# Kernel optimization log

Hardware: AMD Instinct MI355X
Metric: run time of the kernel (lower is better)

## Reference

```python
import jax, jax.numpy as jnp
import numpy as np

DIM = 128
HEADS = DIM // 8      # mala uses dim//8 heads
HEAD_DIM = 8
HID = int(DIM * 2.66) # 340
B, H, W = 8, 128, 128


def _ln(x, w, b):
    # WithBias LayerNorm over channel dim of NCHW (per-pixel)
    mu = jnp.mean(x, axis=1, keepdims=True)
    var = jnp.mean((x - mu) ** 2, axis=1, keepdims=True)
    return (x - mu) / jnp.sqrt(var + 1e-5) * w[None, :, None, None] + b[None, :, None, None]


def _conv1x1(x, w):
    return jnp.einsum('bchw,oc->bohw', x, w)


def _dwconv(x, w, pad):
    return jax.lax.conv_general_dilated(
        x, w, (1, 1), ((pad, pad), (pad, pad)),
        dimension_numbers=('NCHW', 'OIHW', 'NCHW'),
        feature_group_count=x.shape[1])


def _rope(h, w, head_dim, dtype):
    angle = 1.0 / 10000 ** jnp.linspace(0.0, 1.0, head_dim // 4, dtype=dtype)
    angle = jnp.repeat(angle, 2)                                  # [d/2]
    ih = jnp.arange(h, dtype=dtype)[:, None] * angle[None, :]     # [h, d/2]
    iw = jnp.arange(w, dtype=dtype)[:, None] * angle[None, :]     # [w, d/2]
    d2 = head_dim // 2
    sin = jnp.concatenate([jnp.broadcast_to(jnp.sin(ih)[:, None, :], (h, w, d2)),
                           jnp.broadcast_to(jnp.sin(iw)[None, :, :], (h, w, d2))], -1)
    cos = jnp.concatenate([jnp.broadcast_to(jnp.cos(ih)[:, None, :], (h, w, d2)),
                           jnp.broadcast_to(jnp.cos(iw)[None, :, :], (h, w, d2))], -1)
    return sin.reshape(h * w, head_dim), cos.reshape(h * w, head_dim)


def _rot2(x):
    x1 = x[..., 0::2]
    x2 = x[..., 1::2]
    return jnp.stack([-x2, x1], axis=-1).reshape(x.shape)


def _theta_shift(x, sin, cos):
    return x * cos + _rot2(x) * sin


def setup_inputs() -> dict:
    key = jax.random.key(0)
    ks = jax.random.split(key, 8)
    f = jnp.float32
    return {
        'x': jax.random.normal(ks[0], (B, DIM, H, W), f),
        'ln1_w': jnp.ones((DIM,), f), 'ln1_b': jnp.zeros((DIM,), f),
        'qkvo_w': jax.random.normal(ks[1], (4 * DIM, DIM), f) * (DIM ** -0.5),
        'qkvo_b': jnp.zeros((4 * DIM,), f),
        'lepe_w': jax.random.normal(ks[2], (DIM, 1, 5, 5), f) * 0.2,
        'lepe_b': jnp.zeros((DIM,), f),
        'proj_w': jax.random.normal(ks[3], (DIM, DIM), f) * (DIM ** -0.5),
        'proj_b': jnp.zeros((DIM,), f),
        'ln2_w': jnp.ones((DIM,), f), 'ln2_b': jnp.zeros((DIM,), f),
        'ffn_in_w': jax.random.normal(ks[4], (2 * HID, DIM), f) * (DIM ** -0.5),
        'ffn_dw_w': jax.random.normal(ks[5], (2 * HID, 1, 3, 3), f) * (1.0 / 3.0),
        'ffn_out_w': jax.random.normal(ks[6], (DIM, HID), f) * (HID ** -0.5),
    }


def reference(x, ln1_w, ln1_b, qkvo_w, qkvo_b, lepe_w, lepe_b, proj_w, proj_b,
              ln2_w, ln2_b, ffn_in_w, ffn_dw_w, ffn_out_w):
    Bx, C, Hh, Ww = x.shape
    L = Hh * Ww
    n, d = HEADS, HEAD_DIM
    scale = d ** -0.5

    # --- MALA branch ---
    xn = _ln(x, ln1_w, ln1_b)
    sin, cos = _rope(Hh, Ww, d, x.dtype)
    qkvo = _conv1x1(xn, qkvo_w) + qkvo_b[None, :, None, None]       # [B,4C,H,W]
    qkv, o = qkvo[:, :3 * C], qkvo[:, 3 * C:]
    lepe = _dwconv(qkv[:, 2 * C:], lepe_w, 2) + lepe_b[None, :, None, None]
    t = qkv.reshape(Bx, 3, n, d, L).transpose(1, 0, 2, 4, 3)         # [3,B,n,L,d]
    q = jax.nn.elu(t[0]) + 1.0
    k = jax.nn.elu(t[1]) + 1.0
    v = t[2]
    # z = q @ mean_l(k)^T * scale  (pre-RoPE features)
    z = jnp.einsum('bnld,bnd->bnl', q, jnp.mean(k, axis=2))[..., None] * scale  # [B,n,L,1]
    q = _theta_shift(q, sin, cos)
    k = _theta_shift(k, sin, cos)
    kv = jnp.einsum('bnld,bnle->bnde', k, v) * (scale / L)           # [B,n,d,d]
    res = jnp.einsum('bnld,bnde->bnle', q, kv) * (1.0 + 1.0 / (z + 1e-6)) \
          - z * jnp.mean(v, axis=2, keepdims=True)                   # [B,n,L,d]
    res = res.transpose(0, 1, 3, 2).reshape(Bx, C, Hh, Ww) + lepe
    attn = _conv1x1(res * o, proj_w) + proj_b[None, :, None, None]
    x = x + attn

    # --- gated dwconv FFN ---
    xn2 = _ln(x, ln2_w, ln2_b)
    p = _dwconv(_conv1x1(xn2, ffn_in_w), ffn_dw_w, 1)                # [B,2*HID,H,W]
    x1, x2 = p[:, :HID], p[:, HID:]
    x = x + _conv1x1(jax.nn.gelu(x1, approximate=False) * x2, ffn_out_w)
    return x
```

## Files before the change

kernel.cpp:

```cpp
#include <hip/hip_runtime.h>

#define LSP 16384
#define NBATCH 8
#define NPOS (NBATCH*LSP)
#define NHID 340
#define ATT_SCALE 0.35355339059327373f

#define OFF_A        0ULL
#define OFF_B        33554432ULL
#define OFF_GT2      79691776ULL
#define OFF_C        100663296ULL
#define OFF_PART     134217728ULL
#define OFF_STATS    134381568ULL
#define OFF_SIN      134422528ULL
#define OFF_COS      134946816ULL
#define OFF_WQ       135471104ULL
#define OFF_WQO      135602176ULL
#define OFF_QOB      135667712ULL
#define OFF_WP       135668736ULL
#define OFF_WFI      135701504ULL
#define OFF_WFO      135881728ULL
#define WS_NEEDED    135971840ULL

typedef __attribute__((ext_vector_type(8))) short short8;
typedef __attribute__((ext_vector_type(4))) float floatx4;

__device__ __forceinline__ float bf2f(unsigned short u){
  union { unsigned int i; float f; } c; c.i = ((unsigned int)u) << 16; return c.f;
}
__device__ __forceinline__ unsigned short f2bf(float f){
  union { float f; unsigned int i; } c; c.f = f;
  unsigned int r = c.i + 0x7fffu + ((c.i >> 16) & 1u);
  return (unsigned short)(r >> 16);
}

__device__ __forceinline__ void load_row12(const unsigned short* p, float* r){
  const unsigned int* q = (const unsigned int*)p;
  #pragma unroll
  for (int i=0;i<6;i++){
    unsigned int u = q[i];
    r[2*i]   = bf2f((unsigned short)(u & 0xffffu));
    r[2*i+1] = bf2f((unsigned short)(u >> 16));
  }
}

__device__ __forceinline__ void load_row10(const unsigned short* base, float* r){
  short8 B = *(const short8*)(base + 8);
  r[0] = bf2f(base[7]);
  #pragma unroll
  for (int i=0;i<8;i++) r[1+i] = bf2f((unsigned short)B[i]);
  r[9] = bf2f(base[16]);
}

__global__ void rope_kernel(float* __restrict__ sin_t, float* __restrict__ cos_t){
  int l = blockIdx.x*256 + threadIdx.x;
  if (l >= LSP) return;
  int h = l >> 7, w = l & 127;
  float s0 = sinf((float)h),        c0 = cosf((float)h);
  float s1 = sinf((float)h*1e-4f),  c1 = cosf((float)h*1e-4f);
  float s2 = sinf((float)w),        c2 = cosf((float)w);
  float s3 = sinf((float)w*1e-4f),  c3 = cosf((float)w*1e-4f);
  float* sp = sin_t + l*8; float* cp = cos_t + l*8;
  sp[0]=s0; sp[1]=s0; sp[2]=s1; sp[3]=s1; sp[4]=s2; sp[5]=s2; sp[6]=s3; sp[7]=s3;
  cp[0]=c0; cp[1]=c0; cp[2]=c1; cp[3]=c1; cp[4]=c2; cp[5]=c2; cp[6]=c3; cp[7]=c3;
}

__global__ void wconv_kernel(const float* __restrict__ src, unsigned short* __restrict__ dst,
                             int O, int K, int OP, int KP){
  int i = blockIdx.x*256 + threadIdx.x;
  if (i >= OP*KP) return;
  int o = i / KP, k = i - o*KP;
  float v = (o < O && k < K) ? src[o*K + k] : 0.f;
  dst[i] = f2bf(v);
}

__global__ void reorder_qo_kernel(const float* __restrict__ qkvo_w, const float* __restrict__ qkvo_b,
                                  unsigned short* __restrict__ wqo, float* __restrict__ qo_bias){
  int i = blockIdx.x*256 + threadIdx.x;
  if (i < 256){
    qo_bias[i] = qkvo_b[(i < 128) ? i : i + 256];
  }
  if (i >= 256*128) return;
  int o = i >> 7, k = i & 127;
  int srow = (o < 128) ? o : o + 256;
  wqo[i] = f2bf(qkvo_w[srow*128 + k]);
}

__launch_bounds__(256)
__global__ void ln_kernel(const float* __restrict__ x, const float* __restrict__ gam,
                          const float* __restrict__ bet, unsigned short* __restrict__ out_t){
  __shared__ float ps[2][128], pq[2][128];
  __shared__ unsigned short tile[128*132];
  int t = threadIdx.x;
  int pidx = t & 127;
  int half = t >> 7;
  int p0 = blockIdx.x*128;
  int p = p0 + pidx;
  int b = p >> 14, l = p & 16383;
  const float* xb = x + (((size_t)b) << 21) + (((size_t)(half*64)) << 14) + l;
  float vals[64];
  float s = 0.f, sq = 0.f;
  #pragma unroll
  for (int c = 0; c < 64; c++){
    float v = xb[(size_t)c << 14];
    vals[c] = v;
    s += v; sq += v*v;
  }
  ps[half][pidx] = s; pq[half][pidx] = sq;
  __syncthreads();
  float S = ps[0][pidx] + ps[1][pidx];
  float Q = pq[0][pidx] + pq[1][pidx];
  float mu = S * 0.0078125f;
  float var = Q * 0.0078125f - mu*mu;
  float rstd = rsqrtf(var + 1e-5f);
  #pragma unroll
  for (int c0 = 0; c0 < 64; c0 += 8){
    short8 vv;
    #pragma unroll
    for (int i = 0; i < 8; i++){
      int c = c0 + i;
      int cg = half*64 + c;
      vv[i] = (short)f2bf((vals[c] - mu) * rstd * gam[cg] + bet[cg]);
    }
    *(short8*)&tile[pidx*132 + half*64 + c0] = vv;
  }
  __syncthreads();
  unsigned short* og = out_t + ((size_t)p0 << 7);
  #pragma unroll
  for (int it = 0; it < 8; it++){
    int idx = it*256 + t;
    int row = idx >> 4;
    int col = (idx & 15) * 8;
    *(short8*)&og[(row << 7) + col] = *(const short8*)&tile[row*132 + col];
  }
}

template<int OPAD, int KPAD, int NL, bool HASBIAS, bool RESID, bool OUTBF16>
__launch_bounds__(256)
__global__ void gemm_kernel(const unsigned short* __restrict__ in_t,
                            const unsigned short* __restrict__ wb,
                            const float* __restrict__ bias,
                            const float* __restrict__ resid,
                            void* __restrict__ outp){
  constexpr int KS = KPAD / 32;
  constexpr int SBYTES = OUTBF16 ? (64*136*2) : (64*132*4);
  __shared__ __align__(16) unsigned char smem[SBYTES];
  const int t = threadIdx.x;
  const int lane = t & 63;
  const int wv = t >> 6;
  const int lane15 = lane & 15;
  const int quad = lane >> 4;
  const int oc = blockIdx.y;

  #pragma unroll 1
  for (int tl = 0; tl < NL; tl++){
    const int l0 = (blockIdx.x * NL + tl) * 128;
    const int b = l0 >> 14;
    const int lloc0 = l0 & 16383;

    short8 fb[2][KS];
    {
      const unsigned short* base = in_t + ((size_t)(l0 + wv*32 + lane15)) * KPAD + quad*8;
      #pragma unroll
      for (int nt = 0; nt < 2; nt++){
        #pragma unroll
        for (int ks = 0; ks < KS; ks++)
          fb[nt][ks] = *(const short8*)(base + (size_t)nt*16*KPAD + ks*32);
      }
    }
    floatx4 acc[4][2];
    #pragma unroll
    for (int mt=0; mt<4; mt++)
      #pragma unroll
      for (int nt=0; nt<2; nt++)
        acc[mt][nt] = (floatx4){0.f,0.f,0.f,0.f};
    #pragma unroll
    for (int ks = 0; ks < KS; ks++){
      short8 fa[4];
      const unsigned short* wrow = wb + ((size_t)(oc*64 + lane15)) * KPAD + ks*32 + quad*8;
      #pragma unroll
      for (int mt=0; mt<4; mt++)
        fa[mt] = *(const short8*)(wrow + (size_t)mt*16*KPAD);
      #pragma unroll
      for (int mt=0; mt<4; mt++)
        #pragma unroll
        for (int nt=0; nt<2; nt++)
          acc[mt][nt] = __builtin_amdgcn_mfma_f32_16x16x32_bf16(fa[mt], fb[nt][ks], acc[mt][nt], 0, 0, 0);
    }

    if (tl) __syncthreads();

    if (OUTBF16){
      unsigned short* cs = (unsigned short*)smem;
      #pragma unroll
      for (int mt=0; mt<4; mt++)
        #pragma unroll
        for (int nt=0; nt<2; nt++)
          #pragma unroll
          for (int r=0; r<4; r++){
            const int o = mt*16 + quad*4 + r;
            float v = acc[mt][nt][r];
            if (HASBIAS) v += bias[oc*64 + o];
            cs[o*136 + wv*32 + nt*16 + lane15] = f2bf(v);
          }
      __syncthreads();
      unsigned short* og = (unsigned short*)outp;
      #pragma unroll
      for (int j=0; j<4; j++){
        int idx = j*256 + t;
        int row = idx >> 4;
        int col = (idx & 15) * 8;
        short8 v = *(const short8*)&cs[row*136 + col];
        *(short8*)&og[(((size_t)(b*OPAD + oc*64 + row)) << 14) + lloc0 + col] = v;
      }
    } else {
      float* cf = (float*)smem;
      #pragma unroll
      for (int mt=0; mt<4; mt++)
        #pragma unroll
        for (int nt=0; nt<2; nt++)
          #pragma unroll
          for (int r=0; r<4; r++){
            const int o = mt*16 + quad*4 + r;
            float v = acc[mt][nt][r];
            if (HASBIAS) v += bias[oc*64 + o];
            cf[o*132 + wv*32 + nt*16 + lane15] = v;
          }
      __syncthreads();
      float* og = (float*)outp;
      #pragma unroll
      for (int j=0; j<8; j++){
        int idx = j*256 + t;
        int row = idx >> 5;
        int col = (idx & 31) * 4;
        floatx4 v = *(const floatx4*)&cf[row*132 + col];
        if (RESID){
          floatx4 rv = *(const floatx4*)(resid + (((size_t)(b*128 + oc*64 + row)) << 14) + lloc0 + col);
          v += rv;
        }
        *(floatx4*)&og[(((size_t)(b*OPAD + oc*64 + row)) << 14) + lloc0 + col] = v;
      }
    }
  }
}

__launch_bounds__(256)
__global__ void ffn_out_gemm(const unsigned short* __restrict__ g,
                             const unsigned short* __restrict__ wb,
                             float* __restrict__ outp){
  __shared__ __align__(16) unsigned char smem[64*132*4];
  const int t = threadIdx.x;
  const int l0 = blockIdx.x * 128;
  const int b = l0 >> 14;
  const int lloc0 = l0 & 16383;
  const int lane = t & 63;
  const int wv = t >> 6;
  const int lane15 = lane & 15;
  const int quad = lane >> 4;
  const int oc = blockIdx.y;
  const int jj = t >> 3;
  const int c8 = t & 7;

  auto stage = [&](int s, int bufi){
    unsigned short* buf = (unsigned short*)(smem + bufi*10240);
    int j = s*32 + jj;
    const unsigned short* src = g + (((size_t)(b*NHID + j)) << 14) + lloc0;
    #pragma unroll
    for (int cc=0; cc<2; cc++){
      int c = c8 + cc*8;
      short8 v = (short8){0,0,0,0,0,0,0,0};
      if (j < NHID) v = *(const short8*)(src + c*8);
      #pragma unroll
      for (int e=0; e<8; e++)
        buf[(c*8+e)*40 + jj] = (unsigned short)v[e];
    }
  };

  floatx4 acc[4][2];
  #pragma unroll
  for (int mt=0; mt<4; mt++)
    #pragma unroll
    for (int nt=0; nt<2; nt++)
      acc[mt][nt] = (floatx4){0.f,0.f,0.f,0.f};

  stage(0, 0);
  #pragma unroll 1
  for (int s=0; s<11; s++){
    __syncthreads();
    if (s < 10) stage(s+1, (s+1)&1);
    const unsigned short* cur = (const unsigned short*)(smem + (s&1)*10240);
    short8 fbv[2];
    #pragma unroll
    for (int nt=0; nt<2; nt++)
      fbv[nt] = *(const short8*)&cur[(wv*32 + nt*16 + lane15)*40 + quad*8];
    const unsigned short* wrow = wb + ((size_t)(oc*64 + lane15))*352 + s*32 + quad*8;
    short8 fa[4];
    #pragma unroll
    for (int mt=0; mt<4; mt++)
      fa[mt] = *(const short8*)(wrow + (size_t)mt*16*352);
    #pragma unroll
    for (int mt=0; mt<4; mt++)
      #pragma unroll
      for (int nt=0; nt<2; nt++)
        acc[mt][nt] = __builtin_amdgcn_mfma_f32_16x16x32_bf16(fa[mt], fbv[nt], acc[mt][nt], 0, 0, 0);
  }
  __syncthreads();
  float* cf = (float*)smem;
  #pragma unroll
  for (int mt=0; mt<4; mt++)
    #pragma unroll
    for (int nt=0; nt<2; nt++)
      #pragma unroll
      for (int r=0; r<4; r++){
        const int o = mt*16 + quad*4 + r;
        cf[o*132 + wv*32 + nt*16 + lane15] = acc[mt][nt][r];
      }
  __syncthreads();
  #pragma unroll
  for (int j=0; j<8; j++){
    int idx = j*256 + t;
    int row = idx >> 5;
    int col = (idx & 31) * 4;
    floatx4 v = *(const floatx4*)&cf[row*132 + col];
    size_t oi = (((size_t)(b*128 + oc*64 + row)) << 14) + lloc0 + col;
    floatx4 rv = *(const floatx4*)&outp[oi];
    v += rv;
    *(floatx4*)&outp[oi] = v;
  }
}

__launch_bounds__(256)
__global__ void lepe_kernel(const unsigned short* __restrict__ kv,
                            const float* __restrict__ lw, const float* __restrict__ lb,
                            unsigned short* __restrict__ lepe){
  __shared__ unsigned short lds[132*136];
  int bc = blockIdx.x;
  int b = bc >> 7, c = bc & 127;
  int t = threadIdx.x;
  #pragma unroll
  for (int i = t; i < 132*136/8; i += 256)
    *(short8*)(lds + i*8) = (short8){0,0,0,0,0,0,0,0};
  __syncthreads();
  int band = t >> 4, wi = t & 15, w0 = wi*8;
  const unsigned short* vp = kv + (((size_t)(b*256 + 128 + c)) << 14);
  {
    #pragma unroll
    for (int it = 0; it < 8; it++){
      int hh = band + it*16;
      short8 v = *(const short8*)(vp + (hh<<7) + w0);
      unsigned int* dst = (unsigned int*)&lds[(hh+2)*136 + w0 + 2];
      union { short8 s; unsigned int u[4]; } cv; cv.s = v;
      #pragma unroll
      for (int q=0;q<4;q++) dst[q] = cv.u[q];
    }
  }
  float wt[25];
  #pragma unroll
  for (int i=0;i<25;i++) wt[i] = lw[c*25 + i];
  float bias = lb[c];
  __syncthreads();
  int h0 = band*8;
  float win[5][12];
  #pragma unroll
  for (int m=0;m<4;m++) load_row12(&lds[(h0+m)*136 + w0], win[m]);
  unsigned short* outp = lepe + ((size_t)bc << 14);
  #pragma unroll
  for (int s=0;s<8;s++){
    load_row12(&lds[(h0+4+s)*136 + w0], win[(4+s)%5]);
    short8 ov;
    #pragma unroll
    for (int j=0;j<8;j++){
      float acc = bias;
      #pragma unroll
      for (int dy=0;dy<5;dy++){
        const float* r = win[(s+dy)%5];
        #pragma unroll
        for (int dx=0;dx<5;dx++) acc += wt[dy*5+dx]*r[j+dx];
      }
      ov[j] = (short)f2bf(acc);
    }
    *(short8*)(outp + (h0+s)*128 + w0) = ov;
  }
}

__launch_bounds__(256)
__global__ void attn_partial(const unsigned short* __restrict__ kv,
                             const float* __restrict__ sin_t, const float* __restrict__ cos_t,
                             float* __restrict__ partials){
  int pair = blockIdx.x >> 3;
  int chunk = blockIdx.x & 7;
  int b = pair >> 4, hd = pair & 15;
  const unsigned short* kb = kv + (((size_t)(b*256 + hd*8)) << 14);
  const unsigned short* vb = kb + ((size_t)128 << 14);
  float red[80];
  #pragma unroll
  for (int i=0;i<80;i++) red[i]=0.f;
  int l0 = chunk*2048;
  for (int li=0; li<8; li++){
    int l = l0 + li*256 + threadIdx.x;
    float k[8], v[8], ks[8];
    #pragma unroll
    for (int e=0;e<8;e++){
      float t = bf2f(kb[((size_t)e<<14)+l]);
      k[e] = t>0.f ? t+1.f : __expf(t);
      v[e] = bf2f(vb[((size_t)e<<14)+l]);
      red[e]   += k[e];
      red[8+e] += v[e];
    }
    const float* sp = sin_t + l*8;
    const float* cp = cos_t + l*8;
    #pragma unroll
    for (int j=0;j<4;j++){
      float x1=k[2*j], x2=k[2*j+1];
      ks[2*j]   = x1*cp[2*j]   - x2*sp[2*j];
      ks[2*j+1] = x2*cp[2*j+1] + x1*sp[2*j+1];
    }
    #pragma unroll
    for (int d=0; d<8; d++)
      #pragma unroll
      for (int e=0;e<8;e++)
        red[16 + d*8 + e] += ks[d]*v[e];
  }
  #pragma unroll
  for (int off=32; off>0; off>>=1){
    #pragma unroll
    for (int i=0;i<80;i++)
      red[i] += __shfl_down(red[i], off);
  }
  __shared__ float lds[4][80];
  int lane = threadIdx.x & 63, wv = threadIdx.x >> 6;
  if (lane==0){
    #pragma unroll
    for (int i=0;i<80;i++) lds[wv][i] = red[i];
  }
  __syncthreads();
  if (threadIdx.x < 80){
    float s = lds[0][threadIdx.x]+lds[1][threadIdx.x]+lds[2][threadIdx.x]+lds[3][threadIdx.x];
    partials[(size_t)blockIdx.x*80 + threadIdx.x] = s;
  }
}

__global__ void attn_combine(const float* __restrict__ partials, float* __restrict__ stats){
  int i = blockIdx.x*256 + threadIdx.x;
  if (i >= 128*80) return;
  int pair = i / 80, idx = i - pair*80;
  float s = 0.f;
  #pragma unroll
  for (int cc=0; cc<8; cc++)
    s += partials[(size_t)(pair*8+cc)*80+idx];
  s *= (idx < 16) ? (1.f/LSP) : (ATT_SCALE/LSP);
  stats[i] = s;
}

__launch_bounds__(256)
__global__ void attn_apply_kernel(const unsigned short* __restrict__ qo,
                                  const unsigned short* __restrict__ lepe,
                                  const float* __restrict__ stats,
                                  const float* __restrict__ sin_t,
                                  const float* __restrict__ cos_t,
                                  unsigned short* __restrict__ resg_t){
  __shared__ float st[8*80];
  __shared__ unsigned short tile[256*66];
  int p0 = blockIdx.x * 256;
  int b = p0 >> 14;
  int hg = blockIdx.y;
  for (int i = threadIdx.x; i < 8*80; i += 256) st[i] = stats[b*16*80 + hg*8*80 + i];
  __syncthreads();
  int t = threadIdx.x;
  int p = p0 + t;
  int l = p & 16383;
  float sv[8], cv[8];
  {
    const float* sp = sin_t + l*8;
    const float* cp = cos_t + l*8;
    #pragma unroll
    for (int i=0;i<8;i++){ sv[i]=sp[i]; cv[i]=cp[i]; }
  }
  #pragma unroll 1
  for (int hd8=0; hd8<8; hd8++){
    int hd = hg*8 + hd8;
    const float* S = st + hd8*80;
    const unsigned short* qb = qo + (((size_t)(b*256 + hd*8)) << 14) + l;
    const unsigned short* ob = qb + ((size_t)128 << 14);
    const unsigned short* lb = lepe + (((size_t)(b*128 + hd*8)) << 14) + l;
    float q[8];
    #pragma unroll
    for (int e=0;e<8;e++){
      float tq = bf2f(qb[(size_t)e<<14]);
      q[e] = tq > 0.f ? tq + 1.f : __expf(tq);
    }
    float z = 0.f;
    #pragma unroll
    for (int e=0;e<8;e++) z += q[e]*S[e];
    z *= ATT_SCALE;
    float qs[8];
    #pragma unroll
    for (int jj=0;jj<4;jj++){
      float x1=q[2*jj], x2=q[2*jj+1];
      qs[2*jj]   = x1*cv[2*jj]   - x2*sv[2*jj];
      qs[2*jj+1] = x2*cv[2*jj+1] + x1*sv[2*jj+1];
    }
    float fac = 1.f + 1.f/(z + 1e-6f);
    short8 vv;
    #pragma unroll
    for (int e=0;e<8;e++){
      float r = 0.f;
      #pragma unroll
      for (int d=0; d<8; d++) r += qs[d]*S[16 + d*8 + e];
      r = r*fac - z*S[8+e];
      float val = (r + bf2f(lb[(size_t)e<<14])) * bf2f(ob[(size_t)e<<14]);
      vv[e] = (short)f2bf(val);
    }
    *(short8*)&tile[t*66 + hd8*8] = vv;
  }
  __syncthreads();
  unsigned short* og = resg_t + ((size_t)p0 << 7) + hg*64;
  #pragma unroll
  for (int it = 0; it < 8; it++){
    int idx = it*256 + t;
    int row = idx >> 3;
    int col = (idx & 7) * 8;
    *(short8*)&og[(row << 7) + col] = *(const short8*)&tile[row*66 + col];
  }
}

#define FPL (66*144)
__launch_bounds__(256)
__global__ void ffn_dwg_kernel(const unsigned short* __restrict__ p,
                               const float* __restrict__ dw,
                               unsigned short* __restrict__ g){
  __shared__ unsigned short lds[2*FPL];
  int bid = blockIdx.x;
  int jc = bid % NHID;
  int rest = bid / NHID;
  int bb = rest & 1;
  int half = rest >> 1;
  int t = threadIdx.x;
  #pragma unroll
  for (int i = t; i < 2*FPL/8; i += 256)
    *(short8*)(lds + i*8) = (short8){0,0,0,0,0,0,0,0};
  __syncthreads();
  int band = t >> 4, wi = t & 15, w0 = wi*8;
  #pragma unroll
  for (int pl=0; pl<2; pl++){
    const unsigned short* src = p + (((size_t)(bb*704 + jc + pl*NHID)) << 14);
    #pragma unroll
    for (int it=0; it<5; it++){
      int r_idx = it*16 + band;
      if (r_idx < 66){
        int h = half*64 - 1 + r_idx;
        if ((unsigned)h < 128u){
          short8 v = *(const short8*)(src + (h<<7) + w0);
          *(short8*)(&lds[pl*FPL + r_idx*144 + w0 + 8]) = v;
        }
      }
    }
  }
  float w1[9], w2[9];
  #pragma unroll
  for (int i=0;i<9;i++){ w1[i] = dw[jc*9 + i]; w2[i] = dw[(jc+NHID)*9 + i]; }
  __syncthreads();
  int rb = band*4;
  float r1[3][10], r2[3][10];
  #pragma unroll
  for (int m=0;m<2;m++){
    load_row10(&lds[(rb+m)*144 + w0], r1[m]);
    load_row10(&lds[FPL + (rb+m)*144 + w0], r2[m]);
  }
  unsigned short* outp = g + (((size_t)(bb*NHID + jc)) << 14);
  #pragma unroll
  for (int s=0;s<4;s++){
    load_row10(&lds[(rb+2+s)*144 + w0], r1[(2+s)%3]);
    load_row10(&lds[FPL + (rb+2+s)*144 + w0], r2[(2+s)%3]);
    int h = half*64 + rb + s;
    short8 ov;
    #pragma unroll
    for (int j=0;j<8;j++){
      float c1 = 0.f, c2 = 0.f;
      #pragma unroll
      for (int dy=0;dy<3;dy++){
        const float* a = r1[(s+dy)%3];
        const float* bpt = r2[(s+dy)%3];
        #pragma unroll
        for (int dx=0;dx<3;dx++){
          c1 += w1[dy*3+dx]*a[j+dx];
          c2 += w2[dy*3+dx]*bpt[j+dx];
        }
      }
      float ge = 0.5f*c1*(1.f + erff(c1*0.70710678118654752f));
      ov[j] = (short)f2bf(ge*c2);
    }
    *(short8*)(outp + h*128 + w0) = ov;
  }
}

extern "C" void kernel_launch(void* const* d_in, const int* in_sizes, int n_in,
                              void* d_out, int out_size, void* d_ws, size_t ws_size,
                              hipStream_t stream){
  (void)in_sizes; (void)n_in; (void)out_size;
  if (ws_size < WS_NEEDED) return;
  const float* x        = (const float*)d_in[0];
  const float* ln1_w    = (const float*)d_in[1];
  const float* ln1_b    = (const float*)d_in[2];
  const float* qkvo_w   = (const float*)d_in[3];
  const float* qkvo_b   = (const float*)d_in[4];
  const float* lepe_w   = (const float*)d_in[5];
  const float* lepe_b   = (const float*)d_in[6];
  const float* proj_w   = (const float*)d_in[7];
  const float* proj_b   = (const float*)d_in[8];
  const float* ln2_w    = (const float*)d_in[9];
  const float* ln2_b    = (const float*)d_in[10];
  const float* ffn_in_w = (const float*)d_in[11];
  const float* ffn_dw_w = (const float*)d_in[12];
  const float* ffn_out_w= (const float*)d_in[13];

  char* ws = (char*)d_ws;
  unsigned short* bufA   = (unsigned short*)(ws + OFF_A);
  unsigned short* bufB   = (unsigned short*)(ws + OFF_B);
  unsigned short* lepe   = (unsigned short*)(ws + OFF_C);
  unsigned short* gbuf   = (unsigned short*)(ws + OFF_C);
  float* partials        = (float*)(ws + OFF_GT2);
  float* stats           = (float*)(ws + OFF_STATS);
  float* sin_t           = (float*)(ws + OFF_SIN);
  float* cos_t           = (float*)(ws + OFF_COS);
  unsigned short* wq     = (unsigned short*)(ws + OFF_WQ);
  unsigned short* wqo    = (unsigned short*)(ws + OFF_WQO);
  float* qo_bias         = (float*)(ws + OFF_QOB);
  unsigned short* wp     = (unsigned short*)(ws + OFF_WP);
  unsigned short* wfi    = (unsigned short*)(ws + OFF_WFI);
  unsigned short* wfo    = (unsigned short*)(ws + OFF_WFO);
  const unsigned short* wkv = wq + 128*128;

  float* out_f = (float*)d_out;
  dim3 blk(256);
  hipLaunchKernelGGL(rope_kernel, dim3(64), blk, 0, stream, sin_t, cos_t);
  hipLaunchKernelGGL(wconv_kernel, dim3((512*128)/256), blk, 0, stream, qkvo_w, wq, 512,128,512,128);
  hipLaunchKernelGGL(reorder_qo_kernel, dim3((256*128)/256), blk, 0, stream, qkvo_w, qkvo_b, wqo, qo_bias);
  hipLaunchKernelGGL(wconv_kernel, dim3((128*128)/256), blk, 0, stream, proj_w, wp, 128,128,128,128);
  hipLaunchKernelGGL(wconv_kernel, dim3((704*128)/256), blk, 0, stream, ffn_in_w, wfi, 680,128,704,128);
  hipLaunchKernelGGL(wconv_kernel, dim3((128*352)/256), blk, 0, stream, ffn_out_w, wfo, 128,340,128,352);

  hipLaunchKernelGGL(ln_kernel, dim3(1024), blk, 0, stream, x, ln1_w, ln1_b, bufA);
  hipLaunchKernelGGL((gemm_kernel<256,128,2,true,false,true>), dim3(512,4), blk, 0, stream,
                     bufA, wkv, qkvo_b + 128, (const float*)nullptr, (void*)bufB);
  hipLaunchKernelGGL(lepe_kernel, dim3(1024), blk, 0, stream, bufB, lepe_w, lepe_b, lepe);
  hipLaunchKernelGGL(attn_partial, dim3(1024), blk, 0, stream, bufB, sin_t, cos_t, partials);
  hipLaunchKernelGGL(attn_combine, dim3(40), blk, 0, stream, partials, stats);
  hipLaunchKernelGGL((gemm_kernel<256,128,2,true,false,true>), dim3(512,4), blk, 0, stream,
                     bufA, wqo, qo_bias, (const float*)nullptr, (void*)bufB);
  hipLaunchKernelGGL(attn_apply_kernel, dim3(512,2), blk, 0, stream, bufB, lepe, stats, sin_t, cos_t, bufA);
  hipLaunchKernelGGL((gemm_kernel<128,128,1,true,true,false>), dim3(1024,2), blk, 0, stream,
                     bufA, wp, proj_b, x, (void*)out_f);

  hipLaunchKernelGGL(ln_kernel, dim3(1024), blk, 0, stream, out_f, ln2_w, ln2_b, bufA);
  for (int bp = 0; bp < 4; bp++){
    const unsigned short* xin = bufA + (size_t)bp*32768*128;
    float* outp = out_f + (size_t)bp*2*128*16384;
    hipLaunchKernelGGL((gemm_kernel<704,128,2,false,false,true>), dim3(128,11), blk, 0, stream,
                       xin, wfi, (const float*)nullptr, (const float*)nullptr, (void*)bufB);
    hipLaunchKernelGGL(ffn_dwg_kernel, dim3(1360), blk, 0, stream, bufB, ffn_dw_w, gbuf);
    hipLaunchKernelGGL(ffn_out_gemm, dim3(256,2), blk, 0, stream, gbuf, wfo, outp);
  }
}
```

Measured before the change: 685.3 us.

## Fuse proj GEMM with residual add and LayerNorm2; retune QKV GEMM tiling

Adds a proj_ln_kernel that computes the proj 1x1 conv, adds the bias and the residual, writes x1, and computes LayerNorm2 statistics in-block, emitting the bf16 normalized output directly. This removes the separate ln_kernel pass over the fp32 out tensor. It also changes the two 256-row GEMMs to a different tile parameter (4 instead of 2) with half the grid, and reuses the output buffer as scratch for the attention partials. The risks are in-place aliasing, since bufA is both input and output of the fused kernel, and a variance computed as E[x^2]-mu^2.

New measurement: 670.5 us. -2.2%, faster.

```diff
diff --git a/kernel.cpp b/kernel.cpp
--- a/kernel.cpp
+++ b/kernel.cpp
@@ -8,9 +8,7 @@
 
 #define OFF_A        0ULL
 #define OFF_B        33554432ULL
-#define OFF_GT2      79691776ULL
 #define OFF_C        100663296ULL
-#define OFF_PART     134217728ULL
 #define OFF_STATS    134381568ULL
 #define OFF_SIN      134422528ULL
 #define OFF_COS      134946816ULL
@@ -241,6 +239,127 @@
         *(floatx4*)&og[(((size_t)(b*OPAD + oc*64 + row)) << 14) + lloc0 + col] = v;
       }
     }
+  }
+}
+
+__launch_bounds__(256)
+__global__ void proj_ln_kernel(const unsigned short* __restrict__ in_t,
+                               const unsigned short* __restrict__ wb,
+                               const float* __restrict__ bias,
+                               const float* __restrict__ resid,
+                               const float* __restrict__ gam,
+                               const float* __restrict__ bet,
+                               float* __restrict__ x1out,
+                               unsigned short* __restrict__ xn2out){
+  __shared__ __align__(16) unsigned char smem[128*132*4];
+  __shared__ float ssum[8][128], qsum[8][128];
+  __shared__ float muA[128], rsA[128];
+  const int t = threadIdx.x;
+  const int l0 = blockIdx.x * 128;
+  const int b = l0 >> 14;
+  const int lloc0 = l0 & 16383;
+  const int lane = t & 63;
+  const int wv = t >> 6;
+  const int lane15 = lane & 15;
+  const int quad = lane >> 4;
+
+  short8 fb[2][4];
+  {
+    const unsigned short* base = in_t + ((size_t)(l0 + wv*32 + lane15)) * 128 + quad*8;
+    #pragma unroll
+    for (int nt = 0; nt < 2; nt++)
+      #pragma unroll
+      for (int ks = 0; ks < 4; ks++)
+        fb[nt][ks] = *(const short8*)(base + (size_t)nt*16*128 + ks*32);
+  }
+
+  float* cf = (float*)smem;
+  #pragma unroll 1
+  for (int oc = 0; oc < 2; oc++){
+    floatx4 acc[4][2];
+    #pragma unroll
+    for (int mt=0; mt<4; mt++)
+      #pragma unroll
+      for (int nt=0; nt<2; nt++)
+        acc[mt][nt] = (floatx4){0.f,0.f,0.f,0.f};
+    #pragma unroll
+    for (int ks = 0; ks < 4; ks++){
+      short8 fa[4];
+      const unsigned short* wrow = wb + ((size_t)(oc*64 + lane15)) * 128 + ks*32 + quad*8;
+      #pragma unroll
+      for (int mt=0; mt<4; mt++)
+        fa[mt] = *(const short8*)(wrow + (size_t)mt*16*128);
+      #pragma unroll
+      for (int mt=0; mt<4; mt++)
+        #pragma unroll
+        for (int nt=0; nt<2; nt++)
+          acc[mt][nt] = __builtin_amdgcn_mfma_f32_16x16x32_bf16(fa[mt], fb[nt][ks], acc[mt][nt], 0, 0, 0);
+    }
+    #pragma unroll
+    for (int mt=0; mt<4; mt++)
+      #pragma unroll
+      for (int nt=0; nt<2; nt++)
+        #pragma unroll
+        for (int r=0; r<4; r++){
+          const int o = oc*64 + mt*16 + quad*4 + r;
+          cf[o*132 + wv*32 + nt*16 + lane15] = acc[mt][nt][r] + bias[o];
+        }
+  }
+  __syncthreads();
+
+  const int colg = (t & 31) * 4;
+  const int rsub = t >> 5;
+  floatx4 x1r[16];
+  floatx4 s4 = (floatx4){0.f,0.f,0.f,0.f};
+  floatx4 q4 = (floatx4){0.f,0.f,0.f,0.f};
+  #pragma unroll
+  for (int j=0; j<16; j++){
+    int row = j*8 + rsub;
+    floatx4 v = *(const floatx4*)&cf[row*132 + colg];
+    floatx4 rv = *(const floatx4*)&resid[(((size_t)(b*128 + row)) << 14) + lloc0 + colg];
+    v += rv;
+    *(floatx4*)&x1out[(((size_t)(b*128 + row)) << 14) + lloc0 + colg] = v;
+    x1r[j] = v;
+    s4 += v;
+    q4 += v*v;
+  }
+  #pragma unroll
+  for (int e=0; e<4; e++){
+    ssum[rsub][colg+e] = s4[e];
+    qsum[rsub][colg+e] = q4[e];
+  }
+  __syncthreads();
+  if (t < 128){
+    float S = 0.f, Q = 0.f;
+    #pragma unroll
+    for (int g=0; g<8; g++){ S += ssum[g][t]; Q += qsum[g][t]; }
+    float mu = S * 0.0078125f;
+    float var = Q * 0.0078125f - mu*mu;
+    muA[t] = mu;
+    rsA[t] = rsqrtf(var + 1e-5f);
+  }
+  __syncthreads();
+
+  unsigned short* tb = (unsigned short*)smem;
+  #pragma unroll
+  for (int j=0; j<16; j++){
+    int row = j*8 + rsub;
+    float ga = gam[row], be = bet[row];
+    #pragma unroll
+    for (int e=0; e<4; e++){
+      int p = colg + e;
+      float xv = (x1r[j][e] - muA[p]) * rsA[p] * ga + be;
+      tb[p*136 + row] = f2bf(xv);
+    }
+  }
+  __syncthreads();
+  unsigned short* og = xn2out + ((size_t)l0 << 7);
+  #pragma unroll
+  for (int it = 0; it < 8; it++){
+    int idx = it*256 + t;
+    int prow = idx >> 4;
+    int ccol = (idx & 15) * 8;
+    *(short8*)&og[(prow << 7) + ccol] = *(const short8*)&tb[prow*136 + ccol];
   }
 }
 
@@ -619,7 +738,6 @@
   unsigned short* bufB   = (unsigned short*)(ws + OFF_B);
   unsigned short* lepe   = (unsigned short*)(ws + OFF_C);
   unsigned short* gbuf   = (unsigned short*)(ws + OFF_C);
-  float* partials        = (float*)(ws + OFF_GT2);
   float* stats           = (float*)(ws + OFF_STATS);
   float* sin_t           = (float*)(ws + OFF_SIN);
   float* cos_t           = (float*)(ws + OFF_COS);
@@ -632,6 +750,7 @@
   const unsigned short* wkv = wq + 128*128;
 
   float* out_f = (float*)d_out;
+  float* partials = out_f;
   dim3 blk(256);
   hipLaunchKernelGGL(rope_kernel, dim3(64), blk, 0, stream, sin_t, cos_t);
   hipLaunchKernelGGL(wconv_kernel, dim3((512*128)/256), blk, 0, stream, qkvo_w, wq, 512,128,512,128);
@@ -641,18 +760,17 @@
   hipLaunchKernelGGL(wconv_kernel, dim3((128*352)/256), blk, 0, stream, ffn_out_w, wfo, 128,340,128,352);
 
   hipLaunchKernelGGL(ln_kernel, dim3(1024), blk, 0, stream, x, ln1_w, ln1_b, bufA);
-  hipLaunchKernelGGL((gemm_kernel<256,128,2,true,false,true>), dim3(512,4), blk, 0, stream,
+  hipLaunchKernelGGL((gemm_kernel<256,128,4,true,false,true>), dim3(256,4), blk, 0, stream,
                      bufA, wkv, qkvo_b + 128, (const float*)nullptr, (void*)bufB);
   hipLaunchKernelGGL(lepe_kernel, dim3(1024), blk, 0, stream, bufB, lepe_w, lepe_b, lepe);
   hipLaunchKernelGGL(attn_partial, dim3(1024), blk, 0, stream, bufB, sin_t, cos_t, partials);
   hipLaunchKernelGGL(attn_combine, dim3(40), blk, 0, stream, partials, stats);
-  hipLaunchKernelGGL((gemm_kernel<256,128,2,true,false,true>), dim3(512,4), blk, 0, stream,
+  hipLaunchKernelGGL((gemm_kernel<256,128,4,true,false,true>), dim3(256,4), blk, 0, stream,
                      bufA, wqo, qo_bias, (const float*)nullptr, (void*)bufB);
   hipLaunchKernelGGL(attn_apply_kernel, dim3(512,2), blk, 0, stream, bufB, lepe, stats, sin_t, cos_t, bufA);
-  hipLaunchKernelGGL((gemm_kernel<128,128,1,true,true,false>), dim3(1024,2), blk, 0, stream,
-                     bufA, wp, proj_b, x, (void*)out_f);
-
-  hipLaunchKernelGGL(ln_kernel, dim3(1024), blk, 0, stream, out_f, ln2_w, ln2_b, bufA);
+  hipLaunchKernelGGL(proj_ln_kernel, dim3(1024), blk, 0, stream,
+                     bufA, wp, proj_b, x, ln2_w, ln2_b, out_f, bufA);
+
   for (int bp = 0; bp < 4; bp++){
     const unsigned short* xin = bufA + (size_t)bp*32768*128;
     float* outp = out_f + (size_t)bp*2*128*16384;
```
